# Optimization experiments

Measured on AMD Instinct MI355X. Metric: run time of the kernel, lower is better.

Reference implementation:

```python
import jax, jax.numpy as jnp
from jax import lax
import numpy as np

K = 31      # avg_pool2d kernel_size
PAD = 15    # avg_pool2d padding
EPS = 1.0
GAMMA = 5.0


def _box_avg(x):
    # Separable 31x31 box filter, stride 1, zero padding 15,
    # count_include_pad=True (PyTorch default) -> always divide by K*K.
    s = lax.reduce_window(x, 0.0, lax.add, (1, 1, K, 1), (1, 1, 1, 1),
                          [(0, 0), (0, 0), (PAD, PAD), (0, 0)])
    s = lax.reduce_window(s, 0.0, lax.add, (1, 1, 1, K), (1, 1, 1, 1),
                          [(0, 0), (0, 0), (0, 0), (PAD, PAD)])
    return s / (K * K)


def setup_inputs() -> dict:
    key = jax.random.key(0)
    k1, k2 = jax.random.split(key)
    shape = (64, 1, 512, 512)  # [B, C, H, W]
    inp = jax.random.uniform(k1, shape, dtype=jnp.float32)
    tgt = jax.random.uniform(k2, shape, dtype=jnp.float32)
    return {"input": inp, "target": tgt}


def reference(input, target):
    weight = 1.0 + GAMMA * jnp.abs(_box_avg(target) - target)
    intersection = jnp.sum(input * target * weight)
    denom = jnp.sum(input * weight) + jnp.sum(target * weight)
    dice = (2.0 * intersection + EPS) / (denom + EPS)
    return 1.0 - dice
```

## Files before the change

kernel.cpp:

```cpp
#include <hip/hip_runtime.h>


#define BATCH 64
#define H     512
#define W     512
#define PADR  15
#define RBAND 64
#define RING  38
#define NBLK  (BATCH * (H / RBAND))

__global__ __launch_bounds__(256) void fused_kernel(const float* __restrict__ tgt,
                                                    const float* __restrict__ inp,
                                                    float4* __restrict__ partials) {
    const int tid  = threadIdx.x;
    const int lane = tid & 63;
    const int wv   = tid >> 6;
    const int blk  = blockIdx.x;
    const int band = blk & 7;
    const int b    = blk >> 3;
    const int R0   = band * RBAND;
    const float* timg = tgt + (size_t)b * H * W;
    const float* iimg = inp + (size_t)b * H * W;

    __shared__ __align__(16) float ring[RING * W];

    const int col0 = lane * 8;
    const int ofsE = lane * 4;
    const int ofsO = 256 + lane * 4;

    for (int k = 0; k < 10; ++k) {
        const int r_off = wv + 4 * k;
        if (r_off < RING) {
            const int row = R0 - 15 + r_off;
            float4 v0 = make_float4(0.f, 0.f, 0.f, 0.f), v1 = v0;
            if (row >= 0 && row < H) {
                v0 = *(const float4*)(timg + (size_t)row * W + col0);
                v1 = *(const float4*)(timg + (size_t)row * W + col0 + 4);
            }
            const int slot = (row + RING) % RING;
            *(float4*)&ring[slot * W + ofsE] = v0;
            *(float4*)&ring[slot * W + ofsO] = v1;
        }
    }
    __syncthreads();

    const float mL1 = (lane >= 1) ? 1.f : 0.f;
    const float mR1 = (lane <= 62) ? 1.f : 0.f;
    const float mL2 = (lane >= 2) ? 1.f : 0.f;
    const float mR2 = (lane <= 61) ? 1.f : 0.f;

    float vr[8];
    #pragma unroll
    for (int k = 0; k < 8; ++k) vr[k] = 0.f;
    #pragma unroll
    for (int jj = -PADR; jj <= PADR; ++jj) {
        const int rr = R0 + wv + jj;
        const int sl = ((rr + RING) % RING) * W;
        const float4 a = *(const float4*)&ring[sl + ofsE];
        const float4 c = *(const float4*)&ring[sl + ofsO];
        vr[0] += a.x; vr[1] += a.y; vr[2] += a.z; vr[3] += a.w;
        vr[4] += c.x; vr[5] += c.y; vr[6] += c.z; vr[7] += c.w;
    }

    const float inv = 1.0f / 961.0f;
    float aI = 0.f, aA = 0.f, aB = 0.f;

    for (int j = 0; j < 16; ++j) {
        const int h = R0 + 4 * j + wv;

        float4 pf0 = make_float4(0.f, 0.f, 0.f, 0.f), pf1 = pf0;
        const int prow = R0 + 4 * j + 23 + wv;
        if (j < 14 && prow < H) {
            pf0 = *(const float4*)(timg + (size_t)prow * W + col0);
            pf1 = *(const float4*)(timg + (size_t)prow * W + col0 + 4);
        }
        const float4 i0 = *(const float4*)(iimg + (size_t)h * W + col0);
        const float4 i1 = *(const float4*)(iimg + (size_t)h * W + col0 + 4);

        const int slC = (h % RING) * W;
        const float4 t0 = *(const float4*)&ring[slC + ofsE];
        const float4 t1 = *(const float4*)&ring[slC + ofsO];

        float4 adv0[4], adv1[4], sb0[4], sb1[4];
        if (j < 15) {
            #pragma unroll
            for (int q = 0; q < 4; ++q) {
                const int slA = ((h + 16 + q) % RING) * W;
                const int slS = (((h - 15 + q) + RING) % RING) * W;
                adv0[q] = *(const float4*)&ring[slA + ofsE];
                adv1[q] = *(const float4*)&ring[slA + ofsO];
                sb0[q]  = *(const float4*)&ring[slS + ofsE];
                sb1[q]  = *(const float4*)&ring[slS + ofsO];
            }
        }

        const float p1 = vr[0];
        const float p2 = p1 + vr[1];
        const float p3 = p2 + vr[2];
        const float p4 = p3 + vr[3];
        const float p5 = p4 + vr[4];
        const float p6 = p5 + vr[5];
        const float p7 = p6 + vr[6];
        const float s  = p7 + vr[7];
        const float f1 = s - p1, f2 = s - p2, f3 = s - p3, f4 = s - p4;
        const float f5 = s - p5, f6 = s - p6, f7 = s - p7;

        const float sL1 = __shfl_up(s, 1, 64);
        const float sR1 = __shfl_down(s, 1, 64);
        const float g1 = __shfl_up(f1, 2, 64);
        const float g2 = __shfl_up(f2, 2, 64);
        const float g3 = __shfl_up(f3, 2, 64);
        const float g4 = __shfl_up(f4, 2, 64);
        const float g5 = __shfl_up(f5, 2, 64);
        const float g6 = __shfl_up(f6, 2, 64);
        const float g7 = __shfl_up(f7, 2, 64);
        const float q1 = __shfl_down(p1, 2, 64);
        const float q2 = __shfl_down(p2, 2, 64);
        const float q3 = __shfl_down(p3, 2, 64);
        const float q4 = __shfl_down(p4, 2, 64);
        const float q5 = __shfl_down(p5, 2, 64);
        const float q6 = __shfl_down(p6, 2, 64);
        const float q7 = __shfl_down(p7, 2, 64);

        const float S3 = fmaf(mL1, sL1, fmaf(mR1, sR1, s));
        float win[8];
        win[0] = fmaf(mL2, g1, S3);
        win[1] = fmaf(mL2, g2, fmaf(mR2, q1, S3));
        win[2] = fmaf(mL2, g3, fmaf(mR2, q2, S3));
        win[3] = fmaf(mL2, g4, fmaf(mR2, q3, S3));
        win[4] = fmaf(mL2, g5, fmaf(mR2, q4, S3));
        win[5] = fmaf(mL2, g6, fmaf(mR2, q5, S3));
        win[6] = fmaf(mL2, g7, fmaf(mR2, q6, S3));
        win[7] = fmaf(mR2, q7, S3);

        const float tv[8] = {t0.x, t0.y, t0.z, t0.w, t1.x, t1.y, t1.z, t1.w};
        const float iv[8] = {i0.x, i0.y, i0.z, i0.w, i1.x, i1.y, i1.z, i1.w};

        #pragma unroll
        for (int k = 0; k < 8; ++k) {
            const float wgt = fmaf(5.0f, fabsf(fmaf(win[k], inv, -tv[k])), 1.0f);
            aI += iv[k] * tv[k] * wgt;
            aA += iv[k] * wgt;
            aB += tv[k] * wgt;
        }

        if (j < 15) {
            #pragma unroll
            for (int q = 0; q < 4; ++q) {
                vr[0] += adv0[q].x - sb0[q].x; vr[1] += adv0[q].y - sb0[q].y;
                vr[2] += adv0[q].z - sb0[q].z; vr[3] += adv0[q].w - sb0[q].w;
                vr[4] += adv1[q].x - sb1[q].x; vr[5] += adv1[q].y - sb1[q].y;
                vr[6] += adv1[q].z - sb1[q].z; vr[7] += adv1[q].w - sb1[q].w;
            }
        }
        __syncthreads();

        if (j < 14) {
            const int sl = (prow % RING) * W;
            *(float4*)&ring[sl + ofsE] = pf0;
            *(float4*)&ring[sl + ofsO] = pf1;
        }
        __syncthreads();
    }

    #pragma unroll
    for (int off = 32; off > 0; off >>= 1) {
        aI += __shfl_down(aI, off, 64);
        aA += __shfl_down(aA, off, 64);
        aB += __shfl_down(aB, off, 64);
    }
    if (lane == 0) { ring[wv] = aI; ring[8 + wv] = aA; ring[16 + wv] = aB; }
    __syncthreads();
    if (tid == 0) {
        float4 o;
        o.x = ring[0] + ring[1] + ring[2] + ring[3];
        o.y = ring[8] + ring[9] + ring[10] + ring[11];
        o.z = ring[16] + ring[17] + ring[18] + ring[19];
        o.w = 0.f;
        partials[blk] = o;
    }
}

__global__ __launch_bounds__(512) void reduce_kernel(const float4* __restrict__ partials,
                                                     float* __restrict__ out) {
    const int tid = threadIdx.x;
    const float4 v = partials[tid];
    float aI = v.x, aA = v.y, aB = v.z;
    #pragma unroll
    for (int off = 32; off > 0; off >>= 1) {
        aI += __shfl_down(aI, off, 64);
        aA += __shfl_down(aA, off, 64);
        aB += __shfl_down(aB, off, 64);
    }
    __shared__ float s[3][8];
    const int wvx = tid >> 6, ln = tid & 63;
    if (ln == 0) { s[0][wvx] = aI; s[1][wvx] = aA; s[2][wvx] = aB; }
    __syncthreads();
    if (tid == 0) {
        float I = 0.f, A = 0.f, Bv = 0.f;
        #pragma unroll
        for (int k = 0; k < 8; ++k) { I += s[0][k]; A += s[1][k]; Bv += s[2][k]; }
        out[0] = 1.0f - (2.0f * I + 1.0f) / (A + Bv + 1.0f);
    }
}

extern "C" void kernel_launch(void* const* d_in, const int* in_sizes, int n_in,
                              void* d_out, int out_size, void* d_ws, size_t ws_size,
                              hipStream_t stream) {
    const float* inp = (const float*)d_in[0];
    const float* tgt = (const float*)d_in[1];
    float* out = (float*)d_out;

    float4* partials = (float4*)d_ws;

    fused_kernel<<<NBLK, 256, 0, stream>>>(tgt, inp, partials);
    reduce_kernel<<<1, 512, 0, stream>>>(partials, out);
}
```

Measured before the change: 150.2 us.

## Store target ring in bf16 LDS and halve row band per block

The shared ring buffer of target rows is packed as bf16 pairs, which halves LDS usage and allows more resident blocks (launch bounds now request 4). Each block covers 32 rows instead of 64, doubling the block count, and the reduce kernel is widened to match. The aim is higher occupancy and latency hiding. The cost is larger relative halo reloads and bf16 rounding of target values in both the box filter and the weighted sums, which could break accuracy tolerance.

```diff
diff --git a/kernel.cpp b/kernel.cpp
--- a/kernel.cpp
+++ b/kernel.cpp
@@ -1,45 +1,55 @@
 #include <hip/hip_runtime.h>
+#include <hip/hip_bf16.h>
 
 
 #define BATCH 64
 #define H     512
 #define W     512
 #define PADR  15
-#define RBAND 64
+#define RBAND 32
 #define RING  38
 #define NBLK  (BATCH * (H / RBAND))
 
-__global__ __launch_bounds__(256) void fused_kernel(const float* __restrict__ tgt,
-                                                    const float* __restrict__ inp,
-                                                    float4* __restrict__ partials) {
+static __device__ __forceinline__ unsigned pack2(float e, float o) {
+    __hip_bfloat162 h = __float22bfloat162_rn(make_float2(e, o));
+    unsigned u; __builtin_memcpy(&u, &h, 4); return u;
+}
+static __device__ __forceinline__ float2 unpk(unsigned u) {
+    return make_float2(__uint_as_float(u << 16),
+                       __uint_as_float(u & 0xffff0000u));
+}
+
+__global__ __launch_bounds__(256, 4) void fused_kernel(const float* __restrict__ tgt,
+                                                       const float* __restrict__ inp,
+                                                       float4* __restrict__ partials) {
     const int tid  = threadIdx.x;
     const int lane = tid & 63;
     const int wv   = tid >> 6;
     const int blk  = blockIdx.x;
-    const int band = blk & 7;
-    const int b    = blk >> 3;
+    const int band = blk & 15;
+    const int b    = blk >> 4;
     const int R0   = band * RBAND;
     const float* timg = tgt + (size_t)b * H * W;
     const float* iimg = inp + (size_t)b * H * W;
 
-    __shared__ __align__(16) float ring[RING * W];
+    __shared__ __align__(16) unsigned ring[RING * 256];
 
     const int col0 = lane * 8;
-    const int ofsE = lane * 4;
-    const int ofsO = 256 + lane * 4;
+    const int ofs  = lane * 4;
 
     for (int k = 0; k < 10; ++k) {
         const int r_off = wv + 4 * k;
         if (r_off < RING) {
             const int row = R0 - 15 + r_off;
             float4 v0 = make_float4(0.f, 0.f, 0.f, 0.f), v1 = v0;
-            if (row >= 0 && row < H) {
+            if (row >= 0) {
                 v0 = *(const float4*)(timg + (size_t)row * W + col0);
                 v1 = *(const float4*)(timg + (size_t)row * W + col0 + 4);
             }
-            const int slot = (row + RING) % RING;
-            *(float4*)&ring[slot * W + ofsE] = v0;
-            *(float4*)&ring[slot * W + ofsO] = v1;
+            uint4 u;
+            u.x = pack2(v0.x, v0.y); u.y = pack2(v0.z, v0.w);
+            u.z = pack2(v1.x, v1.y); u.w = pack2(v1.z, v1.w);
+            *(uint4*)&ring[((row + RING) % RING) * 256 + ofs] = u;
         }
     }
     __syncthreads();
@@ -55,42 +65,37 @@
     #pragma unroll
     for (int jj = -PADR; jj <= PADR; ++jj) {
         const int rr = R0 + wv + jj;
-        const int sl = ((rr + RING) % RING) * W;
-        const float4 a = *(const float4*)&ring[sl + ofsE];
-        const float4 c = *(const float4*)&ring[sl + ofsO];
-        vr[0] += a.x; vr[1] += a.y; vr[2] += a.z; vr[3] += a.w;
-        vr[4] += c.x; vr[5] += c.y; vr[6] += c.z; vr[7] += c.w;
+        const uint4 c = *(const uint4*)&ring[((rr + RING) % RING) * 256 + ofs];
+        const float2 e0 = unpk(c.x), e1 = unpk(c.y), e2 = unpk(c.z), e3 = unpk(c.w);
+        vr[0] += e0.x; vr[1] += e0.y; vr[2] += e1.x; vr[3] += e1.y;
+        vr[4] += e2.x; vr[5] += e2.y; vr[6] += e3.x; vr[7] += e3.y;
     }
 
     const float inv = 1.0f / 961.0f;
     float aI = 0.f, aA = 0.f, aB = 0.f;
 
-    for (int j = 0; j < 16; ++j) {
+    for (int j = 0; j < 8; ++j) {
         const int h = R0 + 4 * j + wv;
 
         float4 pf0 = make_float4(0.f, 0.f, 0.f, 0.f), pf1 = pf0;
         const int prow = R0 + 4 * j + 23 + wv;
-        if (j < 14 && prow < H) {
+        if (j < 7 && prow < H) {
             pf0 = *(const float4*)(timg + (size_t)prow * W + col0);
             pf1 = *(const float4*)(timg + (size_t)prow * W + col0 + 4);
         }
         const float4 i0 = *(const float4*)(iimg + (size_t)h * W + col0);
         const float4 i1 = *(const float4*)(iimg + (size_t)h * W + col0 + 4);
 
-        const int slC = (h % RING) * W;
-        const float4 t0 = *(const float4*)&ring[slC + ofsE];
-        const float4 t1 = *(const float4*)&ring[slC + ofsO];
-
-        float4 adv0[4], adv1[4], sb0[4], sb1[4];
-        if (j < 15) {
+        const uint4 tc = *(const uint4*)&ring[(h % RING) * 256 + ofs];
+
+        uint4 ua[4], us[4];
+        if (j < 7) {
             #pragma unroll
             for (int q = 0; q < 4; ++q) {
-                const int slA = ((h + 16 + q) % RING) * W;
-                const int slS = (((h - 15 + q) + RING) % RING) * W;
-                adv0[q] = *(const float4*)&ring[slA + ofsE];
-                adv1[q] = *(const float4*)&ring[slA + ofsO];
-                sb0[q]  = *(const float4*)&ring[slS + ofsE];
-                sb1[q]  = *(const float4*)&ring[slS + ofsO];
+                const int ar = h + 16 + q;
+                ua[q] = (ar < H) ? *(const uint4*)&ring[(ar % RING) * 256 + ofs]
+                                 : make_uint4(0u, 0u, 0u, 0u);
+                us[q] = *(const uint4*)&ring[(((h - 15 + q) + RING) % RING) * 256 + ofs];
             }
         }
 
@@ -133,7 +138,8 @@
         win[6] = fmaf(mL2, g7, fmaf(mR2, q6, S3));
         win[7] = fmaf(mR2, q7, S3);
 
-        const float tv[8] = {t0.x, t0.y, t0.z, t0.w, t1.x, t1.y, t1.z, t1.w};
+        const float2 t0 = unpk(tc.x), t1 = unpk(tc.y), t2 = unpk(tc.z), t3 = unpk(tc.w);
+        const float tv[8] = {t0.x, t0.y, t1.x, t1.y, t2.x, t2.y, t3.x, t3.y};
         const float iv[8] = {i0.x, i0.y, i0.z, i0.w, i1.x, i1.y, i1.z, i1.w};
 
         #pragma unroll
@@ -144,21 +150,26 @@
             aB += tv[k] * wgt;
         }
 
-        if (j < 15) {
+        if (j < 7) {
             #pragma unroll
             for (int q = 0; q < 4; ++q) {
-                vr[0] += adv0[q].x - sb0[q].x; vr[1] += adv0[q].y - sb0[q].y;
-                vr[2] += adv0[q].z - sb0[q].z; vr[3] += adv0[q].w - sb0[q].w;
-                vr[4] += adv1[q].x - sb1[q].x; vr[5] += adv1[q].y - sb1[q].y;
-                vr[6] += adv1[q].z - sb1[q].z; vr[7] += adv1[q].w - sb1[q].w;
+                const float2 a0 = unpk(ua[q].x), a1 = unpk(ua[q].y),
+                             a2 = unpk(ua[q].z), a3 = unpk(ua[q].w);
+                const float2 s0 = unpk(us[q].x), s1 = unpk(us[q].y),
+                             s2 = unpk(us[q].z), s3 = unpk(us[q].w);
+                vr[0] += a0.x - s0.x; vr[1] += a0.y - s0.y;
+                vr[2] += a1.x - s1.x; vr[3] += a1.y - s1.y;
+                vr[4] += a2.x - s2.x; vr[5] += a2.y - s2.y;
+                vr[6] += a3.x - s3.x; vr[7] += a3.y - s3.y;
             }
         }
         __syncthreads();
 
-        if (j < 14) {
-            const int sl = (prow % RING) * W;
-            *(float4*)&ring[sl + ofsE] = pf0;
-            *(float4*)&ring[sl + ofsO] = pf1;
+        if (j < 7 && prow < H) {
+            uint4 u;
+            u.x = pack2(pf0.x, pf0.y); u.y = pack2(pf0.z, pf0.w);
+            u.z = pack2(pf1.x, pf1.y); u.w = pack2(pf1.z, pf1.w);
+            *(uint4*)&ring[(prow % RING) * 256 + ofs] = u;
         }
         __syncthreads();
     }
@@ -169,20 +180,21 @@
         aA += __shfl_down(aA, off, 64);
         aB += __shfl_down(aB, off, 64);
     }
-    if (lane == 0) { ring[wv] = aI; ring[8 + wv] = aA; ring[16 + wv] = aB; }
+    float* rf = (float*)ring;
+    if (lane == 0) { rf[wv] = aI; rf[8 + wv] = aA; rf[16 + wv] = aB; }
     __syncthreads();
     if (tid == 0) {
         float4 o;
-        o.x = ring[0] + ring[1] + ring[2] + ring[3];
-        o.y = ring[8] + ring[9] + ring[10] + ring[11];
-        o.z = ring[16] + ring[17] + ring[18] + ring[19];
+        o.x = rf[0] + rf[1] + rf[2] + rf[3];
+        o.y = rf[8] + rf[9] + rf[10] + rf[11];
+        o.z = rf[16] + rf[17] + rf[18] + rf[19];
         o.w = 0.f;
         partials[blk] = o;
     }
 }
 
-__global__ __launch_bounds__(512) void reduce_kernel(const float4* __restrict__ partials,
-                                                     float* __restrict__ out) {
+__global__ __launch_bounds__(1024) void reduce_kernel(const float4* __restrict__ partials,
+                                                      float* __restrict__ out) {
     const int tid = threadIdx.x;
     const float4 v = partials[tid];
     float aI = v.x, aA = v.y, aB = v.z;
@@ -192,14 +204,14 @@
         aA += __shfl_down(aA, off, 64);
         aB += __shfl_down(aB, off, 64);
     }
-    __shared__ float s[3][8];
+    __shared__ float s[3][16];
     const int wvx = tid >> 6, ln = tid & 63;
     if (ln == 0) { s[0][wvx] = aI; s[1][wvx] = aA; s[2][wvx] = aB; }
     __syncthreads();
     if (tid == 0) {
         float I = 0.f, A = 0.f, Bv = 0.f;
         #pragma unroll
-        for (int k = 0; k < 8; ++k) { I += s[0][k]; A += s[1][k]; Bv += s[2][k]; }
+        for (int k = 0; k < 16; ++k) { I += s[0][k]; A += s[1][k]; Bv += s[2][k]; }
         out[0] = 1.0f - (2.0f * I + 1.0f) / (A + Bv + 1.0f);
     }
 }
@@ -214,5 +226,5 @@
     float4* partials = (float4*)d_ws;
 
     fused_kernel<<<NBLK, 256, 0, stream>>>(tgt, inp, partials);
-    reduce_kernel<<<1, 512, 0, stream>>>(partials, out);
-}
+    reduce_kernel<<<1, 1024, 0, stream>>>(partials, out);
+}
```

Result: no change. 148.2 us (-1.4%).
